# Kernel optimization log

Hardware: AMD Instinct MI355X
Metric: run time of the kernel (lower is better)

Reference implementation:

```python
import jax, jax.numpy as jnp
import numpy as np

N = 50000
E = 500000
D = 128
L = 3
BN_EPS = 1e-5


def setup_inputs() -> dict:
    key = jax.random.key(0)
    ks = jax.random.split(key, 16)

    def xavier(k, shape):
        fan_in, fan_out = shape[-2], shape[-1]
        limit = float(np.sqrt(6.0 / (fan_in + fan_out)))
        return jax.random.uniform(k, shape, jnp.float32, -limit, limit)

    inp = {
        "x": jax.random.randint(ks[0], (N, 2), 0, 3),
        "edge_index": jax.random.randint(ks[1], (2, E), 0, N),
        "edge_attr": jax.random.randint(ks[2], (E, 2), 0, 3),
        # atom embeddings (xavier_uniform like torch init)
        "atom_emb0": xavier(ks[3], (120, D)),
        "atom_emb1": xavier(ks[4], (3, D)),
        # per-layer edge embeddings, stacked over layers
        "edge_emb0": xavier(ks[5], (L, 5, D)),
        "edge_emb1": xavier(ks[6], (L, 3, D)),
        # per-layer MLP: Linear(D, 2D) -> ReLU -> Linear(2D, D)
        "W1": xavier(ks[7], (L, D, 2 * D)),
        "b1": jnp.zeros((L, 2 * D), jnp.float32),
        "W2": xavier(ks[8], (L, 2 * D, D)),
        "b2": jnp.zeros((L, D), jnp.float32),
        # batchnorm affine params
        "gamma": jnp.ones((L, D), jnp.float32),
        "beta": jnp.zeros((L, D), jnp.float32),
    }
    return inp


def reference(x, edge_index, edge_attr, atom_emb0, atom_emb1,
              edge_emb0, edge_emb1, W1, b1, W2, b2, gamma, beta):
    n = x.shape[0]
    num_layer = W1.shape[0]

    # atom embedding: sum of per-attribute embeddings -> [N, D]
    h = atom_emb0[x[:, 0]] + atom_emb1[x[:, 1]]

    # add self loops: src/dst both get arange(N) appended
    loop = jnp.arange(n, dtype=edge_index.dtype)
    src = jnp.concatenate([edge_index[0], loop])  # [E+N]
    dst = jnp.concatenate([edge_index[1], loop])  # [E+N]
    # self-loop edge attr is [4, 0]
    ea0 = jnp.concatenate([edge_attr[:, 0], jnp.full((n,), 4, edge_attr.dtype)])
    ea1 = jnp.concatenate([edge_attr[:, 1], jnp.zeros((n,), edge_attr.dtype)])

    for l in range(num_layer):
        # edge embedding lookup + message = x_j + edge_attr, scatter-add to dst
        eemb = edge_emb0[l][ea0] + edge_emb1[l][ea1]          # [E+N, D]
        msg = h[src] + eemb                                   # gather + add
        aggr = jax.ops.segment_sum(msg, dst, num_segments=n)  # [N, D]
        # MLP update
        hid = jax.nn.relu(aggr @ W1[l] + b1[l])               # [N, 2D]
        out = hid @ W2[l] + b2[l]                             # [N, D]
        # BatchNorm1d (training mode: batch stats, biased variance)
        mean = jnp.mean(out, axis=0)
        var = jnp.mean(jnp.square(out - mean), axis=0)
        out = gamma[l] * (out - mean) * jax.lax.rsqrt(var + BN_EPS) + beta[l]
        # dropout with p=0 is identity; ReLU on all but last layer
        h = out if l == num_layer - 1 else jax.nn.relu(out)
    return h
```

## Files before the change

kernel.cpp:

```cpp
#include <hip/hip_runtime.h>

#define D 128
#define TWO_D 256
#define BN_EPS 1e-5f

typedef __attribute__((ext_vector_type(8))) short bf16x8;
typedef __attribute__((ext_vector_type(4))) float f32x4;
typedef __attribute__((ext_vector_type(4))) unsigned u32x4;

__device__ __forceinline__ float relu_f(float x) { return x > 0.f ? x : 0.f; }

__device__ __forceinline__ unsigned short f2bf(float f) {
    unsigned u = __builtin_bit_cast(unsigned, f);
    return (unsigned short)((u + 0x7FFFu + ((u >> 16) & 1u)) >> 16);
}
__device__ __forceinline__ float bf2f(unsigned s) {
    unsigned u = s << 16;
    return __builtin_bit_cast(float, u);
}
__device__ __forceinline__ unsigned pack2(float a, float b) {
    return (unsigned)f2bf(a) | ((unsigned)f2bf(b) << 16);
}

__device__ __forceinline__ int pad8(int d) { return (d + 7) & ~7; }

__global__ void atom_embed_kernel(const int* __restrict__ x,
                                  const float* __restrict__ emb0,
                                  const float* __restrict__ emb1,
                                  unsigned short* __restrict__ bufA,
                                  unsigned short* __restrict__ bufB, int n) {
    if (blockIdx.x == 0 && threadIdx.x < 64)
        reinterpret_cast<unsigned*>(bufA + (size_t)n * D)[threadIdx.x] = 0u;
    if (blockIdx.x == 1 && threadIdx.x < 64)
        reinterpret_cast<unsigned*>(bufB + (size_t)n * D)[threadIdx.x] = 0u;
    int idx = blockIdx.x * blockDim.x + threadIdx.x;
    if (idx >= n * 32) return;
    int node = idx >> 5;
    int d0 = (idx & 31) << 2;
    int i0 = x[node * 2 + 0];
    int i1 = x[node * 2 + 1];
    const float4 a = *reinterpret_cast<const float4*>(emb0 + (size_t)i0 * D + d0);
    const float4 b = *reinterpret_cast<const float4*>(emb1 + (size_t)i1 * D + d0);
    uint2 v;
    v.x = pack2(a.x + b.x, a.y + b.y);
    v.y = pack2(a.z + b.z, a.w + b.w);
    *reinterpret_cast<uint2*>(bufA + (size_t)node * D + d0) = v;
}

__global__ void hist_kernel(const int* __restrict__ ei, int* __restrict__ counts, int e_cnt) {
    int e = blockIdx.x * blockDim.x + threadIdx.x;
    if (e >= e_cnt) return;
    atomicAdd(counts + ei[e_cnt + e], 1);
}

__global__ __launch_bounds__(256) void bsum_kernel(const int* __restrict__ counts,
                                                   int* __restrict__ bsum, int n) {
    __shared__ int s[256];
    int t = threadIdx.x;
    int idx = blockIdx.x * 256 + t;
    s[t] = (idx < n) ? pad8(counts[idx]) : 0;
    __syncthreads();
    for (int off = 128; off > 0; off >>= 1) {
        if (t < off) s[t] += s[t + off];
        __syncthreads();
    }
    if (t == 0) bsum[blockIdx.x] = s[0];
}

__global__ __launch_bounds__(256) void bscan_kernel(const int* __restrict__ bsum,
                                                    int* __restrict__ bpre,
                                                    int* __restrict__ rpp, int nb, int n) {
    __shared__ int s[256];
    int t = threadIdx.x;
    s[t] = (t < nb) ? bsum[t] : 0;
    __syncthreads();
    for (int off = 1; off < 256; off <<= 1) {
        int v = (t >= off) ? s[t - off] : 0;
        __syncthreads();
        s[t] += v;
        __syncthreads();
    }
    bpre[t] = (t == 0) ? 0 : s[t - 1];
    if (t == 255) rpp[n] = s[255];
}

__global__ __launch_bounds__(256) void scan_apply_kernel(const int* __restrict__ counts,
                                                         const int* __restrict__ bpre,
                                                         int* __restrict__ rpp,
                                                         int* __restrict__ cursor, int n) {
    __shared__ int s[256];
    int t = threadIdx.x;
    int idx = blockIdx.x * 256 + t;
    int c = (idx < n) ? pad8(counts[idx]) : 0;
    s[t] = c;
    __syncthreads();
    for (int off = 1; off < 256; off <<= 1) {
        int v = (t >= off) ? s[t - off] : 0;
        __syncthreads();
        s[t] += v;
        __syncthreads();
    }
    if (idx < n) {
        int excl = bpre[blockIdx.x] + s[t] - c;
        rpp[idx] = excl;
        cursor[idx] = excl;
    }
}

__global__ void fill_kernel(const int* __restrict__ ei, const int* __restrict__ ea,
                            int* __restrict__ cursor,
                            unsigned* __restrict__ ep32, int e_cnt) {
    int e = blockIdx.x * blockDim.x + threadIdx.x;
    if (e >= e_cnt) return;
    int dst = ei[e_cnt + e];
    int src = ei[e];
    int aidx = ea[e * 2 + 0] * 3 + ea[e * 2 + 1];
    int pos = atomicAdd(cursor + dst, 1);
    ep32[pos] = (unsigned)(src & 0x1FFFF) | ((unsigned)aidx << 17);
}

__global__ void convert_kernel(const int* __restrict__ rpp, const int* __restrict__ counts,
                               const unsigned* __restrict__ ep32,
                               unsigned short* __restrict__ ep16,
                               unsigned long long* __restrict__ cnts, int n) {
    int i = blockIdx.x * blockDim.x + threadIdx.x;
    if (i >= n) return;
    const int jb = rpp[i];
    const int deg = counts[i];
    const int pe = pad8(deg);
    unsigned long long c = 0ull;
    int j = 0;
    for (; j < deg; ++j) {
        unsigned v = ep32[jb + j];
        ep16[jb + j] = (unsigned short)(v & 0xFFFFu);
        int a = (int)(v >> 17);
        if (a < 8) c += 1ull << (a * 8);
    }
    for (; j < pe; ++j) ep16[jb + j] = (unsigned short)n;
    cnts[i] = c;
}

__global__ void frag_prep_kernel(const float* __restrict__ W1,
                                 const float* __restrict__ W2,
                                 unsigned short* __restrict__ w1f,
                                 unsigned short* __restrict__ w2f, int Lnum) {
    int tid = blockIdx.x * blockDim.x + threadIdx.x;
    if (tid >= Lnum * 128 * 64) return;
    int l = tid / 8192;
    int rem = tid % 8192;
    int frag = rem / 64;
    int lane = rem % 64;
    int kg = lane >> 4, cl = lane & 15;
    if (frag < 64) {
        int kk = frag >> 4, tn = frag & 15;
        const float* src = W1 + (size_t)l * D * TWO_D;
        int k0 = kk * 32 + kg * 8, col = tn * 16 + cl;
        unsigned short* dst = w1f + (size_t)l * 32768 + ((size_t)frag * 64 + lane) * 8;
        #pragma unroll
        for (int j = 0; j < 8; ++j) dst[j] = f2bf(src[(size_t)(k0 + j) * TWO_D + col]);
    } else {
        int f2 = frag - 64;
        int kk = f2 >> 3, tn = f2 & 7;
        const float* src = W2 + (size_t)l * TWO_D * D;
        int k0 = kk * 32 + kg * 8, col = tn * 16 + cl;
        unsigned short* dst = w2f + (size_t)l * 32768 + ((size_t)f2 * 64 + lane) * 8;
        #pragma unroll
        for (int j = 0; j < 8; ++j) dst[j] = f2bf(src[(size_t)(k0 + j) * D + col]);
    }
}

template<int DO_BN>
__global__ __launch_bounds__(256) void gather_kernel(
    const unsigned short* __restrict__ hbf,
    const float* __restrict__ ee0_l, const float* __restrict__ ee1_l,
    const float* __restrict__ stats_prev,
    const float* __restrict__ gamma_p, const float* __restrict__ beta_p,
    float inv_n,
    const int* __restrict__ rpp, const int* __restrict__ counts,
    const unsigned long long* __restrict__ cnts,
    const unsigned short* __restrict__ ep,
    unsigned short* __restrict__ aggrbf, float* __restrict__ stats_cur, int n) {

    __shared__ float cee[16 * D];
    __shared__ float sbn[2 * D];
    const int t = threadIdx.x;
    if (blockIdx.x == 0) stats_cur[t] = 0.f;
    for (int i = t; i < 16 * D; i += 256) {
        int r = i >> 7, d = i & 127;
        cee[i] = (r < 15) ? ee0_l[(r / 3) * D + d] + ee1_l[(r % 3) * D + d]
                          : ee0_l[4 * D + d] + ee1_l[d];
    }
    if (DO_BN && t < 128) {
        float mean = stats_prev[t] * inv_n;
        float var  = stats_prev[128 + t] * inv_n - mean * mean;
        float sc = gamma_p[t] * rsqrtf(var + BN_EPS);
        sbn[t] = sc;
        sbn[128 + t] = beta_p[t] - mean * sc;
    }
    __syncthreads();

    int node = blockIdx.x * 16 + (t >> 4);
    if (node >= n) return;
    const int d0 = (t & 15) << 3;

    float sc8[8], sh8[8];
    if (DO_BN) {
        #pragma unroll
        for (int j = 0; j < 8; ++j) { sc8[j] = sbn[d0 + j]; sh8[j] = sbn[128 + d0 + j]; }
    }

    const int jb = rpp[node];
    const int deg = counts[node];
    const unsigned long long c0 = cnts[node];
    const int nch = pad8(deg) >> 3;

    float acc[8];
    {
        u32x4 hv = *reinterpret_cast<const u32x4*>(hbf + (size_t)node * D + d0);
        #pragma unroll
        for (int j = 0; j < 4; ++j) {
            float lo = bf2f(hv[j] & 0xffffu), hi = bf2f(hv[j] >> 16);
            if (DO_BN) {
                acc[2 * j]     = relu_f(lo * sc8[2 * j]     + sh8[2 * j]);
                acc[2 * j + 1] = relu_f(hi * sc8[2 * j + 1] + sh8[2 * j + 1]);
            } else {
                acc[2 * j] = lo; acc[2 * j + 1] = hi;
            }
        }
        #pragma unroll
        for (int j = 0; j < 8; ++j) acc[j] += cee[15 * D + d0 + j];
    }

    int csum = 0;
    #pragma unroll
    for (int a = 0; a < 8; ++a) {
        int fc = (int)((c0 >> (a * 8)) & 0xFFull);
        csum += fc;
        float f = (float)fc;
        #pragma unroll
        for (int j = 0; j < 8; ++j) acc[j] += f * cee[a * D + d0 + j];
    }
    {
        float f = (float)(deg - csum);
        #pragma unroll
        for (int j = 0; j < 8; ++j) acc[j] += f * cee[8 * D + d0 + j];
    }

#define ROWLD(s_) (*reinterpret_cast<const u32x4*>(hbf + (size_t)(s_) * D + d0))
#define EACC(q) do { \
        _Pragma("unroll") \
        for (int j_ = 0; j_ < 4; ++j_) { \
            float lo_ = bf2f((q)[j_] & 0xffffu), hi_ = bf2f((q)[j_] >> 16); \
            if (DO_BN) { \
                acc[2 * j_]     += relu_f(lo_ * sc8[2 * j_]     + sh8[2 * j_]); \
                acc[2 * j_ + 1] += relu_f(hi_ * sc8[2 * j_ + 1] + sh8[2 * j_ + 1]); \
            } else { \
                acc[2 * j_] += lo_; acc[2 * j_ + 1] += hi_; \
            } \
        } } while (0)
#define PROC(iv) do { \
        const u32x4 r0_ = ROWLD((iv).x & 0xFFFFu), r1_ = ROWLD((iv).x >> 16); \
        const u32x4 r2_ = ROWLD((iv).y & 0xFFFFu), r3_ = ROWLD((iv).y >> 16); \
        const u32x4 r4_ = ROWLD((iv).z & 0xFFFFu), r5_ = ROWLD((iv).z >> 16); \
        const u32x4 r6_ = ROWLD((iv).w & 0xFFFFu), r7_ = ROWLD((iv).w >> 16); \
        EACC(r0_); EACC(r1_); EACC(r2_); EACC(r3_); \
        EACC(r4_); EACC(r5_); EACC(r6_); EACC(r7_); } while (0)

    if (nch) {
        uint4 iv = *reinterpret_cast<const uint4*>(ep + jb);
        for (int c = 1; c < nch; ++c) {
            uint4 nx = *reinterpret_cast<const uint4*>(ep + jb + 8 * c);
            PROC(iv);
            iv = nx;
        }
        PROC(iv);
    }
#undef ROWLD
#undef EACC
#undef PROC

    if (DO_BN) {
        float np = (float)(pad8(deg) - deg);
        #pragma unroll
        for (int j = 0; j < 8; ++j) acc[j] -= np * relu_f(sh8[j]);
    }

    u32x4 o;
    o[0] = pack2(acc[0], acc[1]);
    o[1] = pack2(acc[2], acc[3]);
    o[2] = pack2(acc[4], acc[5]);
    o[3] = pack2(acc[6], acc[7]);
    __builtin_nontemporal_store(o, reinterpret_cast<u32x4*>(aggrbf + (size_t)node * D + d0));
}

__global__ __launch_bounds__(256) void mlp_mfma_kernel(
    unsigned short* __restrict__ aggrbf,
    const bf16x8* __restrict__ w1f, const bf16x8* __restrict__ w2f,
    const float* __restrict__ b1l, const float* __restrict__ b2l,
    float* __restrict__ outf, float* __restrict__ stats, int n, int final_f32) {

    __shared__ unsigned short hid[32 * TWO_D];
    __shared__ float sred[256];

    const int wave = threadIdx.x >> 6;
    const int lane = threadIdx.x & 63;
    const int arow = lane & 15;
    const int kgrp = lane >> 4;

    bf16x8 W1[4][4];
    #pragma unroll
    for (int kk = 0; kk < 4; ++kk)
        #pragma unroll
        for (int t = 0; t < 4; ++t)
            W1[kk][t] = w1f[(kk * 16 + wave * 4 + t) * 64 + lane];
    bf16x8 W2[8][2];
    #pragma unroll
    for (int kk = 0; kk < 8; ++kk)
        #pragma unroll
        for (int t = 0; t < 2; ++t)
            W2[kk][t] = w2f[(kk * 8 + wave * 2 + t) * 64 + lane];

    float b1v[4], b2v[2];
    #pragma unroll
    for (int t = 0; t < 4; ++t) b1v[t] = b1l[wave * 64 + t * 16 + arow];
    #pragma unroll
    for (int t = 0; t < 2; ++t) b2v[t] = b2l[wave * 32 + t * 16 + arow];

    float ps[2] = {0.f, 0.f}, pq[2] = {0.f, 0.f};

    const int tiles = n >> 4;
    const int npair = (tiles + 1) >> 1;
    for (int p = blockIdx.x; p < npair; p += gridDim.x) {
        const int t0i = 2 * p, t1i = 2 * p + 1;
        const bool has1 = (t1i < tiles);
        const size_t r0 = (size_t)t0i * 16, r1 = (size_t)t1i * 16;

        bf16x8 a0[4], a1[4];
        #pragma unroll
        for (int kk = 0; kk < 4; ++kk)
            a0[kk] = *reinterpret_cast<const bf16x8*>(
                aggrbf + (r0 + arow) * D + kk * 32 + kgrp * 8);
        if (has1) {
            #pragma unroll
            for (int kk = 0; kk < 4; ++kk)
                a1[kk] = *reinterpret_cast<const bf16x8*>(
                    aggrbf + (r1 + arow) * D + kk * 32 + kgrp * 8);
        }

        f32x4 acc1[4];
        #pragma unroll
        for (int t = 0; t < 4; ++t) acc1[t] = (f32x4){0.f, 0.f, 0.f, 0.f};
        #pragma unroll
        for (int kk = 0; kk < 4; ++kk)
            #pragma unroll
            for (int t = 0; t < 4; ++t)
                acc1[t] = __builtin_amdgcn_mfma_f32_16x16x32_bf16(a0[kk], W1[kk][t], acc1[t], 0, 0, 0);

        __syncthreads();
        #pragma unroll
        for (int t = 0; t < 4; ++t) {
            const int cc = wave * 64 + t * 16 + arow;
            #pragma unroll
            for (int r = 0; r < 4; ++r) {
                const int rr = kgrp * 4 + r;
                hid[(rr * TWO_D + cc) ^ ((rr & 7) << 3)] = f2bf(relu_f(acc1[t][r] + b1v[t]));
            }
        }
        if (has1) {
            #pragma unroll
            for (int t = 0; t < 4; ++t) acc1[t] = (f32x4){0.f, 0.f, 0.f, 0.f};
            #pragma unroll
            for (int kk = 0; kk < 4; ++kk)
                #pragma unroll
                for (int t = 0; t < 4; ++t)
                    acc1[t] = __builtin_amdgcn_mfma_f32_16x16x32_bf16(a1[kk], W1[kk][t], acc1[t], 0, 0, 0);
            #pragma unroll
            for (int t = 0; t < 4; ++t) {
                const int cc = wave * 64 + t * 16 + arow;
                #pragma unroll
                for (int r = 0; r < 4; ++r) {
                    const int rr = 16 + kgrp * 4 + r;
                    hid[(rr * TWO_D + cc) ^ ((rr & 7) << 3)] = f2bf(relu_f(acc1[t][r] + b1v[t]));
                }
            }
        }
        __syncthreads();

        {
            f32x4 acc2[2];
            #pragma unroll
            for (int t = 0; t < 2; ++t) acc2[t] = (f32x4){0.f, 0.f, 0.f, 0.f};
            #pragma unroll
            for (int kk = 0; kk < 8; ++kk) {
                bf16x8 a2 = *reinterpret_cast<const bf16x8*>(
                    hid + ((arow * TWO_D + kk * 32 + kgrp * 8) ^ ((arow & 7) << 3)));
                #pragma unroll
                for (int t = 0; t < 2; ++t)
                    acc2[t] = __builtin_amdgcn_mfma_f32_16x16x32_bf16(a2, W2[kk][t], acc2[t], 0, 0, 0);
            }
            #pragma unroll
            for (int t = 0; t < 2; ++t) {
                const int col = wave * 32 + t * 16 + arow;
                #pragma unroll
                for (int r = 0; r < 4; ++r) {
                    float v = acc2[t][r] + b2v[t];
                    if (final_f32) outf[(r0 + kgrp * 4 + r) * D + col] = v;
                    else           aggrbf[(r0 + kgrp * 4 + r) * D + col] = f2bf(v);
                    ps[t] += v; pq[t] += v * v;
                }
            }
        }
        if (has1) {
            f32x4 acc2[2];
            #pragma unroll
            for (int t = 0; t < 2; ++t) acc2[t] = (f32x4){0.f, 0.f, 0.f, 0.f};
            #pragma unroll
            for (int kk = 0; kk < 8; ++kk) {
                bf16x8 a2 = *reinterpret_cast<const bf16x8*>(
                    hid + (((16 + arow) * TWO_D + kk * 32 + kgrp * 8) ^ ((arow & 7) << 3)));
                #pragma unroll
                for (int t = 0; t < 2; ++t)
                    acc2[t] = __builtin_amdgcn_mfma_f32_16x16x32_bf16(a2, W2[kk][t], acc2[t], 0, 0, 0);
            }
            #pragma unroll
            for (int t = 0; t < 2; ++t) {
                const int col = wave * 32 + t * 16 + arow;
                #pragma unroll
                for (int r = 0; r < 4; ++r) {
                    float v = acc2[t][r] + b2v[t];
                    if (final_f32) outf[(r1 + kgrp * 4 + r) * D + col] = v;
                    else           aggrbf[(r1 + kgrp * 4 + r) * D + col] = f2bf(v);
                    ps[t] += v; pq[t] += v * v;
                }
            }
        }
    }

    sred[threadIdx.x] = 0.f;
    __syncthreads();
    #pragma unroll
    for (int t = 0; t < 2; ++t) {
        const int col = wave * 32 + t * 16 + arow;
        atomicAdd(sred + col, ps[t]);
        atomicAdd(sred + 128 + col, pq[t]);
    }
    __syncthreads();
    unsafeAtomicAdd(stats + threadIdx.x, sred[threadIdx.x]);
}

__global__ void bn_apply_final_kernel(const float* __restrict__ out,
                                      const float* __restrict__ stats,
                                      const float* __restrict__ gamma_l,
                                      const float* __restrict__ beta_l,
                                      float inv_n,
                                      float* __restrict__ dst, int n) {
    __shared__ float sbn[2 * D];
    int t = threadIdx.x;
    if (t < 128) {
        float mean = stats[t] * inv_n;
        float var  = stats[128 + t] * inv_n - mean * mean;
        float sc = gamma_l[t] * rsqrtf(var + BN_EPS);
        sbn[t] = sc;
        sbn[128 + t] = beta_l[t] - mean * sc;
    }
    __syncthreads();
    int idx = blockIdx.x * blockDim.x + t;
    if (idx >= n * 32) return;
    int d0 = (idx & 31) << 2;
    float4 v  = *reinterpret_cast<const float4*>(out + (size_t)idx * 4);
    float4 sc = *reinterpret_cast<const float4*>(sbn + d0);
    float4 sh = *reinterpret_cast<const float4*>(sbn + 128 + d0);
    *reinterpret_cast<float4*>(dst + (size_t)idx * 4) =
        make_float4(v.x * sc.x + sh.x, v.y * sc.y + sh.y,
                    v.z * sc.z + sh.z, v.w * sc.w + sh.w);
}

extern "C" void kernel_launch(void* const* d_in, const int* in_sizes, int n_in,
                              void* d_out, int out_size, void* d_ws, size_t ws_size,
                              hipStream_t stream) {
    const int*   x     = (const int*)d_in[0];
    const int*   ei    = (const int*)d_in[1];
    const int*   ea    = (const int*)d_in[2];
    const float* aemb0 = (const float*)d_in[3];
    const float* aemb1 = (const float*)d_in[4];
    const float* eemb0 = (const float*)d_in[5];
    const float* eemb1 = (const float*)d_in[6];
    const float* W1    = (const float*)d_in[7];
    const float* b1    = (const float*)d_in[8];
    const float* W2    = (const float*)d_in[9];
    const float* b2    = (const float*)d_in[10];
    const float* gamma = (const float*)d_in[11];
    const float* beta  = (const float*)d_in[12];

    const int n = in_sizes[0] / 2;
    const int e = in_sizes[1] / 2;
    const int L = in_sizes[8] / TWO_D;
    const float inv_n = 1.0f / (float)n;

    char* ws = (char*)d_ws;
    float* outb = (float*)ws;                      ws += (size_t)n * D * 4;
    unsigned short* bufA = (unsigned short*)ws;    ws += (size_t)(n + 1) * D * 2;
    unsigned short* bufB = (unsigned short*)ws;    ws += (size_t)(n + 1) * D * 2;
    unsigned short* w1f = (unsigned short*)ws;     ws += (size_t)L * 32768 * 2;
    unsigned short* w2f = (unsigned short*)ws;     ws += (size_t)L * 32768 * 2;
    float* statsA = (float*)ws;                    ws += 256 * 4;
    float* statsB = (float*)ws;                    ws += 256 * 4;
    int* counts  = (int*)ws;                       ws += (size_t)n * 4;
    unsigned long long* cnts = (unsigned long long*)ws;  ws += (size_t)n * 8;
    int* rpp     = (int*)ws;                       ws += (size_t)(n + 4) * 4;
    int* cursor  = (int*)ws;                       ws += (size_t)n * 4;
    int* bsum    = (int*)ws;                       ws += 256 * 4;
    int* bpre    = (int*)ws;                       ws += 256 * 4;
    unsigned* ep32 = (unsigned*)ws;                ws += ((size_t)e + 8 * (size_t)n) * 4;
    unsigned short* ep16 = (unsigned short*)ws;

    const int edge_blocks = (e + 255) / 256;
    const int vec_blocks  = (n * 32 + 255) / 256;
    const int node_blocks = (n + 15) / 16;
    const int nb = (n + 255) / 256;

    hipMemsetAsync(counts, 0, (size_t)n * 4, stream);
    hist_kernel<<<edge_blocks, 256, 0, stream>>>(ei, counts, e);
    bsum_kernel<<<nb, 256, 0, stream>>>(counts, bsum, n);
    bscan_kernel<<<1, 256, 0, stream>>>(bsum, bpre, rpp, nb, n);
    scan_apply_kernel<<<nb, 256, 0, stream>>>(counts, bpre, rpp, cursor, n);
    fill_kernel<<<edge_blocks, 256, 0, stream>>>(ei, ea, cursor, ep32, e);
    convert_kernel<<<nb, 256, 0, stream>>>(rpp, counts, ep32, ep16, cnts, n);
    frag_prep_kernel<<<(L * 128 * 64 + 255) / 256, 256, 0, stream>>>(W1, W2, w1f, w2f, L);
    atom_embed_kernel<<<vec_blocks, 256, 0, stream>>>(x, aemb0, aemb1, bufA, bufB, n);

    for (int l = 0; l < L; ++l) {
        const float* ee0_l = eemb0 + (size_t)l * 5 * D;
        const float* ee1_l = eemb1 + (size_t)l * 3 * D;

        unsigned short* src = (l & 1) ? bufB : bufA;
        unsigned short* dst = (l & 1) ? bufA : bufB;
        float* stats_cur  = (l & 1) ? statsB : statsA;
        float* stats_prev = (l & 1) ? statsA : statsB;

        if (l == 0)
            gather_kernel<0><<<node_blocks, 256, 0, stream>>>(
                src, ee0_l, ee1_l, nullptr, nullptr, nullptr, inv_n,
                rpp, counts, cnts, ep16, dst, stats_cur, n);
        else
            gather_kernel<1><<<node_blocks, 256, 0, stream>>>(
                src, ee0_l, ee1_l, stats_prev,
                gamma + (size_t)(l - 1) * D, beta + (size_t)(l - 1) * D, inv_n,
                rpp, counts, cnts, ep16, dst, stats_cur, n);

        mlp_mfma_kernel<<<512, 256, 0, stream>>>(
            dst,
            (const bf16x8*)(w1f + (size_t)l * 32768),
            (const bf16x8*)(w2f + (size_t)l * 32768),
            b1 + (size_t)l * TWO_D, b2 + (size_t)l * D,
            outb, stats_cur, n, (l == L - 1) ? 1 : 0);
    }

    float* stats_last = ((L - 1) & 1) ? statsB : statsA;
    bn_apply_final_kernel<<<vec_blocks, 256, 0, stream>>>(
        outb, stats_last, gamma + (size_t)(L - 1) * D, beta + (size_t)(L - 1) * D,
        inv_n, (float*)d_out, n);
}
```

Before: 258.6 us.

## Prefetch next tile pair's aggregate rows in MLP loop and bound gather occupancy

```diff
diff --git a/kernel.cpp b/kernel.cpp
--- a/kernel.cpp
+++ b/kernel.cpp
@@ -170,7 +170,7 @@
 }
 
 template<int DO_BN>
-__global__ __launch_bounds__(256) void gather_kernel(
+__global__ __launch_bounds__(256, 4) void gather_kernel(
     const unsigned short* __restrict__ hbf,
     const float* __restrict__ ee0_l, const float* __restrict__ ee1_l,
     const float* __restrict__ stats_prev,
@@ -330,22 +330,27 @@
 
     const int tiles = n >> 4;
     const int npair = (tiles + 1) >> 1;
-    for (int p = blockIdx.x; p < npair; p += gridDim.x) {
-        const int t0i = 2 * p, t1i = 2 * p + 1;
-        const bool has1 = (t1i < tiles);
-        const size_t r0 = (size_t)t0i * 16, r1 = (size_t)t1i * 16;
-
-        bf16x8 a0[4], a1[4];
+    const int stride = gridDim.x;
+
+    bf16x8 a0[4], a1[4];
+    int p = blockIdx.x;
+    if (p < npair) {
+        const size_t r0 = (size_t)(2 * p) * 16, r1 = r0 + 16;
         #pragma unroll
         for (int kk = 0; kk < 4; ++kk)
             a0[kk] = *reinterpret_cast<const bf16x8*>(
                 aggrbf + (r0 + arow) * D + kk * 32 + kgrp * 8);
-        if (has1) {
+        if (2 * p + 1 < tiles) {
             #pragma unroll
             for (int kk = 0; kk < 4; ++kk)
                 a1[kk] = *reinterpret_cast<const bf16x8*>(
                     aggrbf + (r1 + arow) * D + kk * 32 + kgrp * 8);
         }
+    }
+
+    for (; p < npair; p += stride) {
+        const bool has1 = (2 * p + 1 < tiles);
+        const size_t r0 = (size_t)(2 * p) * 16, r1 = r0 + 16;
 
         f32x4 acc1[4];
         #pragma unroll
@@ -384,6 +389,24 @@
                 }
             }
         }
+
+        {
+            const int np_ = p + stride;
+            if (np_ < npair) {
+                const size_t nr0 = (size_t)(2 * np_) * 16, nr1 = nr0 + 16;
+                #pragma unroll
+                for (int kk = 0; kk < 4; ++kk)
+                    a0[kk] = *reinterpret_cast<const bf16x8*>(
+                        aggrbf + (nr0 + arow) * D + kk * 32 + kgrp * 8);
+                if (2 * np_ + 1 < tiles) {
+                    #pragma unroll
+                    for (int kk = 0; kk < 4; ++kk)
+                        a1[kk] = *reinterpret_cast<const bf16x8*>(
+                            aggrbf + (nr1 + arow) * D + kk * 32 + kgrp * 8);
+                }
+            }
+        }
+
         __syncthreads();
 
         {
```

Measured after the change: 273.3 us. 5.7% more time.
